# Performance work log

Measured on AMD Instinct MI355X. Metric: run time of the kernel, lower is better.

The kernel has to match this reference:

```python
import jax, jax.numpy as jnp
import numpy as np

BN_EPS = 1e-6
LN_EPS = 1e-5
ROPE_BASE = 10000.0


def rope(x):
    # x: [..., S, d] ; standard half-split rotary embedding, positions 0..S-1
    S, d = x.shape[-2], x.shape[-1]
    half = d // 2
    inv_freq = 1.0 / (ROPE_BASE ** (jnp.arange(half, dtype=jnp.float32) / half))
    ang = jnp.arange(S, dtype=jnp.float32)[:, None] * inv_freq[None, :]  # [S, half]
    cos, sin = jnp.cos(ang), jnp.sin(ang)
    x1, x2 = x[..., :half], x[..., half:]
    return jnp.concatenate([x1 * cos - x2 * sin, x1 * sin + x2 * cos], axis=-1)


def layernorm(x, g, b):
    m = jnp.mean(x, axis=-1, keepdims=True)
    v = jnp.mean((x - m) ** 2, axis=-1, keepdims=True)
    return (x - m) * jax.lax.rsqrt(v + LN_EPS) * g + b


def rms_batchnorm(x, g, b, running):
    # eval-mode RMSBatchNorm1D: normalize by running RMS^2 buffer
    return x * jax.lax.rsqrt(running + BN_EPS) * g + b


def setup_inputs() -> dict:
    B, S, C, H, QD, KD, VD = 4, 2048, 1536, 8, 128, 128, 192
    key = jax.random.key(0)
    ks = jax.random.split(key, 8)
    sc = 0.02
    return {
        'x': jax.random.normal(ks[0], (B, S, C), dtype=jnp.float32),
        'rms_g': jnp.ones((C,), jnp.float32),
        'rms_b': jnp.zeros((C,), jnp.float32),
        'rms_r': jnp.ones((C,), jnp.float32),
        'Wq': jax.random.normal(ks[1], (H * QD, C), jnp.float32) * sc,
        'Wk': jax.random.normal(ks[2], (KD, C), jnp.float32) * sc,
        'Wv': jax.random.normal(ks[3], (VD, C), jnp.float32) * sc,
        'q_g': jnp.ones((QD,), jnp.float32), 'q_b': jnp.zeros((QD,), jnp.float32),
        'k_g': jnp.ones((KD,), jnp.float32), 'k_b': jnp.zeros((KD,), jnp.float32),
        'v_g': jnp.ones((VD,), jnp.float32), 'v_b': jnp.zeros((VD,), jnp.float32),
        'Wo': jax.random.normal(ks[4], (C, H * VD), jnp.float32) * sc,
        'bo': jnp.zeros((C,), jnp.float32),
        'on_g': jnp.ones((C,), jnp.float32),
        'on_b': jnp.zeros((C,), jnp.float32),
        'on_r': jnp.ones((C,), jnp.float32),
    }


def reference(x, rms_g, rms_b, rms_r, Wq, Wk, Wv, q_g, q_b, k_g, k_b, v_g, v_b, Wo, bo, on_g, on_b, on_r):
    B, S, C = x.shape
    H, QD = 8, Wq.shape[0] // 8
    KD, VD = Wk.shape[0], Wv.shape[0]

    xn = rms_batchnorm(x, rms_g, rms_b, rms_r)

    q = (xn @ Wq.T).reshape(B, S, H, QD)       # [B,S,H,QD]
    q = layernorm(q, q_g, q_b)
    k = layernorm(xn @ Wk.T, k_g, k_b)          # [B,S,KD] shared across heads (MQA)
    v = layernorm(xn @ Wv.T, v_g, v_b)          # [B,S,VD]

    # RoPE along sequence dim
    q = rope(jnp.transpose(q, (0, 2, 1, 3)))    # [B,H,S,QD]
    k = rope(k)
    v = rope(v)

    scale = 1.0 / jnp.sqrt(jnp.float32(KD))
    logits = jnp.einsum('bhsc,bSc->bhsS', q, k) * scale   # [B,H,S,S]
    attn = jax.nn.softmax(logits, axis=-1)
    o = jnp.einsum('bhsS,bSc->bshc', attn, v).reshape(B, S, H * VD)

    y = o @ Wo.T + bo                            # [B,S,C]
    y = rms_batchnorm(y, on_g, on_b, on_r)
    # dropout is identity in eval mode
    return y
```

## Files before the change

### kernel.cpp

```cpp
#include <hip/hip_runtime.h>
#include <math.h>

typedef unsigned short u16;
typedef unsigned int   u32;
typedef __attribute__((ext_vector_type(8))) short bf16x8;
typedef __attribute__((ext_vector_type(4))) float f32x4;

#define DEVI static __device__ __forceinline__

constexpr int Bb = 4, Ss = 2048, Cc = 1536, Hh = 8, QD = 128, KD = 128, VD = 192;
constexpr int NTOK = Bb * Ss;
constexpr int NQKV = Hh*QD + KD + VD;
constexpr int NQKV_PAD = 1408;
constexpr float ATTN_SCALE = 0.08838834764831845f;

constexpr size_t OFF_S1  = 0;
constexpr size_t OFF_B1  = OFF_S1 + Cc*4;
constexpr size_t OFF_S2  = OFF_B1 + Cc*4;
constexpr size_t OFF_B2  = OFF_S2 + Cc*4;
constexpr size_t OFF_CT  = 24576;
constexpr size_t OFF_ST  = OFF_CT  + (size_t)Ss*64*4;
constexpr size_t OFF_CTV = OFF_ST  + (size_t)Ss*64*4;
constexpr size_t OFF_STV = OFF_CTV + (size_t)Ss*96*4;
constexpr size_t OFF_WQKV= OFF_STV + (size_t)Ss*96*4;
constexpr size_t OFF_WO  = OFF_WQKV+ (size_t)NQKV_PAD*Cc*2;
constexpr size_t OFF_XN  = OFF_WO  + (size_t)Cc*Cc*2;
constexpr size_t OFF_QKV = OFF_XN  + (size_t)NTOK*Cc*2;
constexpr size_t OFF_Q   = OFF_QKV + (size_t)NTOK*NQKV*2;
constexpr size_t OFF_K   = OFF_Q   + (size_t)NTOK*(Hh*QD)*2;
constexpr size_t OFF_VT  = OFF_K   + (size_t)NTOK*KD*2;

DEVI u16 f2b(float f) {
  union { float f; u32 u; } v; v.f = f;
  u32 r = v.u + 0x7FFFu + ((v.u >> 16) & 1u);
  return (u16)(r >> 16);
}
DEVI float b2f(u16 h) {
  union { u32 u; float f; } v; v.u = ((u32)h) << 16;
  return v.f;
}
DEVI u32 cvtpk(float lo, float hi) {
  u32 r;
  asm("v_cvt_pk_bf16_f32 %0, %1, %2" : "=v"(r) : "v"(lo), "v"(hi));
  return r;
}
DEVI void gload16(const void* g, void* l) {
  __builtin_amdgcn_global_load_lds(g, l, 16, 0, 0);
}
DEVI f32x4 mfma16(bf16x8 a, bf16x8 b, f32x4 c) {
  return __builtin_amdgcn_mfma_f32_16x16x32_bf16(a, b, c, 0, 0, 0);
}

__global__ __launch_bounds__(256) void k_prep_small(
    const float* __restrict__ rms_g, const float* __restrict__ rms_b, const float* __restrict__ rms_r,
    const float* __restrict__ on_g,  const float* __restrict__ on_b,  const float* __restrict__ on_r,
    const float* __restrict__ bo, char* __restrict__ ws)
{
  int i = blockIdx.x * 256 + threadIdx.x;
  float* s1 = (float*)(ws + OFF_S1);
  float* b1 = (float*)(ws + OFF_B1);
  float* s2 = (float*)(ws + OFF_S2);
  float* b2 = (float*)(ws + OFF_B2);
  float* ct = (float*)(ws + OFF_CT);
  float* st = (float*)(ws + OFF_ST);
  float* ctv= (float*)(ws + OFF_CTV);
  float* stv= (float*)(ws + OFF_STV);
  if (i < Cc) {
    float a = rsqrtf(rms_r[i] + 1e-6f) * rms_g[i];
    s1[i] = a; b1[i] = rms_b[i];
    float c = rsqrtf(on_r[i] + 1e-6f) * on_g[i];
    s2[i] = c; b2[i] = bo[i]*c + on_b[i];
  }
  int j = i - Cc;
  if (j >= 0 && j < Ss*64) {
    int s = j >> 6, f = j & 63;
    float invf = expf(-(float)f * (9.210340371976184f / 64.f));
    float ang = (float)s * invf;
    float sn, cs; sincosf(ang, &sn, &cs);
    ct[j] = cs; st[j] = sn;
  }
  int k = j - Ss*64;
  if (k >= 0 && k < Ss*96) {
    int s = k / 96, f = k - s*96;
    float invf = expf(-(float)f * (9.210340371976184f / 96.f));
    float ang = (float)s * invf;
    float sn, cs; sincosf(ang, &sn, &cs);
    ctv[k] = cs; stv[k] = sn;
  }
}

__global__ __launch_bounds__(256) void k_prep_w(
    const float* __restrict__ Wq, const float* __restrict__ Wk, const float* __restrict__ Wv,
    const float* __restrict__ Wo, char* __restrict__ ws)
{
  u16* wqkv = (u16*)(ws + OFF_WQKV);
  u16* wo   = (u16*)(ws + OFF_WO);
  const int total1 = NQKV_PAD * Cc;
  const int total2 = Cc * Cc;
  for (int i = blockIdx.x*256 + threadIdx.x; i < total1 + total2; i += gridDim.x*256) {
    if (i < total1) {
      int r = i / Cc, c = i - r*Cc;
      float v = 0.f;
      if (r < 1024)      v = Wq[(size_t)r*Cc + c];
      else if (r < 1152) v = Wk[(size_t)(r-1024)*Cc + c];
      else if (r < 1344) v = Wv[(size_t)(r-1152)*Cc + c];
      wqkv[i] = f2b(v);
    } else {
      int t2 = i - total1;
      wo[t2] = f2b(Wo[t2]);
    }
  }
}

__global__ __launch_bounds__(256) void k_xn(const float* __restrict__ x, char* __restrict__ ws)
{
  const float* s1 = (const float*)(ws + OFF_S1);
  const float* b1 = (const float*)(ws + OFF_B1);
  u16* xn = (u16*)(ws + OFF_XN);
  int idx = blockIdx.x*256 + threadIdx.x;
  float4 xv = ((const float4*)x)[idx];
  int c = (idx % (Cc/4)) * 4;
  u32 lo = (u32)f2b(xv.x*s1[c]   + b1[c])   | ((u32)f2b(xv.y*s1[c+1] + b1[c+1]) << 16);
  u32 hi = (u32)f2b(xv.z*s1[c+2] + b1[c+2]) | ((u32)f2b(xv.w*s1[c+3] + b1[c+3]) << 16);
  ((uint2*)xn)[idx] = make_uint2(lo, hi);
}

template <bool EPI>
__global__ __launch_bounds__(256) void k_gemm_bt(
    const u16* __restrict__ A, const u16* __restrict__ Bw, void* __restrict__ outp,
    int K, int N_out, const float* __restrict__ s2, const float* __restrict__ b2)
{
  __shared__ u16 a_lds[128*32];
  __shared__ u16 b_lds[128*32];
  const int tid = threadIdx.x;
  const int w = tid >> 6, l = tid & 63;
  const int wr = w >> 1, wc = w & 1;
  const int lr = l & 15, lh = l >> 4;
  const int m0 = blockIdx.y * 128, n0 = blockIdx.x * 128;
  f32x4 acc[4][4] = {};
  const u16* pa = A  + (size_t)(m0 + w*16 + (l>>2))*K + (l&3)*8;
  const u16* pb = Bw + (size_t)(n0 + w*16 + (l>>2))*K + (l&3)*8;
  char* al = (char*)a_lds + w*1024;
  char* bl = (char*)b_lds + w*1024;
  const u16* ar = a_lds + (wr*64 + lr)*32 + lh*8;
  const u16* br = b_lds + (wc*64 + lr)*32 + lh*8;
  for (int k0 = 0; k0 < K; k0 += 32) {
    gload16(pa,                al);
    gload16(pa + (size_t)64*K, al + 4096);
    gload16(pb,                bl);
    gload16(pb + (size_t)64*K, bl + 4096);
    pa += 32; pb += 32;
    __syncthreads();
    bf16x8 af[4], bfr[4];
#pragma unroll
    for (int m = 0; m < 4; m++) af[m]  = *(const bf16x8*)(ar + m*512);
#pragma unroll
    for (int n = 0; n < 4; n++) bfr[n] = *(const bf16x8*)(br + n*512);
#pragma unroll
    for (int m = 0; m < 4; m++)
#pragma unroll
      for (int n = 0; n < 4; n++)
        acc[m][n] = mfma16(af[m], bfr[n], acc[m][n]);
    __syncthreads();
  }
  const int r0 = m0 + wr*64 + lh*4;
  const int c0 = n0 + wc*64 + lr;
#pragma unroll
  for (int m = 0; m < 4; m++) {
#pragma unroll
    for (int n = 0; n < 4; n++) {
      int col = c0 + n*16;
      if (col < N_out) {
#pragma unroll
        for (int r = 0; r < 4; r++) {
          size_t o = (size_t)(r0 + m*16 + r) * N_out + col;
          if (EPI) ((float*)outp)[o] = acc[m][n][r] * s2[col] + b2[col];
          else     ((u16*)outp)[o]   = f2b(acc[m][n][r]);
        }
      }
    }
  }
}

__global__ __launch_bounds__(256) void k_lnrope_qk(
    char* __restrict__ ws,
    const float* __restrict__ q_g, const float* __restrict__ q_b,
    const float* __restrict__ k_g, const float* __restrict__ k_b)
{
  const u16* qkv = (const u16*)(ws + OFF_QKV);
  u16* qo = (u16*)(ws + OFF_Q);
  u16* ko = (u16*)(ws + OFF_K);
  const float* ct = (const float*)(ws + OFF_CT);
  const float* st = (const float*)(ws + OFF_ST);
  const int w = threadIdx.x >> 6, l = threadIdx.x & 63;
  const int rid = blockIdx.x*4 + w;
  const u16* src; u16* dst; const float* g; const float* bb; float osc; int s;
  if (rid < NTOK*Hh) {
    int t = rid >> 3, h = rid & 7;
    s = t & (Ss-1); int b = t >> 11;
    src = qkv + (size_t)t*NQKV + h*QD;
    dst = qo + ((size_t)(b*Hh + h)*Ss + s)*QD;
    g = q_g; bb = q_b; osc = ATTN_SCALE;
  } else {
    int t = rid - NTOK*Hh;
    s = t & (Ss-1);
    src = qkv + (size_t)t*NQKV + Hh*QD;
    dst = ko + (size_t)t*KD;
    g = k_g; bb = k_b; osc = 1.f;
  }
  u32 pk = *(const u32*)(src + 2*l);
  float x0 = b2f((u16)(pk & 0xFFFFu)), x1 = b2f((u16)(pk >> 16));
  float sm = x0 + x1, sq = x0*x0 + x1*x1;
#pragma unroll
  for (int off = 1; off < 64; off <<= 1) { sm += __shfl_xor(sm, off); sq += __shfl_xor(sq, off); }
  float mean = sm * (1.f/128.f);
  float var  = sq * (1.f/128.f) - mean*mean;
  float rstd = rsqrtf(var + 1e-5f);
  int d0 = 2*l;
  float y0 = (x0 - mean)*rstd*g[d0]   + bb[d0];
  float y1 = (x1 - mean)*rstd*g[d0+1] + bb[d0+1];
  float z0 = __shfl_xor(y0, 32);
  float z1 = __shfl_xor(y1, 32);
  int f0 = 2*(l & 31);
  float c0 = ct[s*64 + f0],     s0 = st[s*64 + f0];
  float c1 = ct[s*64 + f0 + 1], s1 = st[s*64 + f0 + 1];
  float o0, o1;
  if (l < 32) { o0 = y0*c0 - z0*s0; o1 = y1*c1 - z1*s1; }
  else        { o0 = z0*s0 + y0*c0; o1 = z1*s1 + y1*c1; }
  o0 *= osc; o1 *= osc;
  *(u32*)(dst + 2*l) = (u32)f2b(o0) | ((u32)f2b(o1) << 16);
}

__global__ __launch_bounds__(256) void k_lnrope_v(
    char* __restrict__ ws, const float* __restrict__ v_g, const float* __restrict__ v_b)
{
  const u16* qkv = (const u16*)(ws + OFF_QKV);
  u16* vo = (u16*)(ws + OFF_VT);
  const float* ct = (const float*)(ws + OFF_CTV);
  const float* st = (const float*)(ws + OFF_STV);
  __shared__ float buf[4][192];
  const int w = threadIdx.x >> 6, l = threadIdx.x & 63;
  const int t = blockIdx.x*4 + w;
  const int s = t & (Ss-1), b = t >> 11;
  const u16* src = qkv + (size_t)t*NQKV + Hh*QD + KD;
  float xs[3]; float sm = 0.f, sq = 0.f;
#pragma unroll
  for (int i2 = 0; i2 < 3; i2++) {
    float xv = b2f(src[l + 64*i2]);
    xs[i2] = xv; buf[w][l + 64*i2] = xv;
    sm += xv; sq += xv*xv;
  }
  __threadfence_block();
#pragma unroll
  for (int off = 1; off < 64; off <<= 1) { sm += __shfl_xor(sm, off); sq += __shfl_xor(sq, off); }
  float mean = sm * (1.f/192.f);
  float var  = sq * (1.f/192.f) - mean*mean;
  float rstd = rsqrtf(var + 1e-5f);
#pragma unroll
  for (int i2 = 0; i2 < 3; i2++) {
    int e = l + 64*i2;
    float val;
    if (e < 96) {
      float x1 = xs[i2], x2 = buf[w][e+96];
      float x1n = (x1-mean)*rstd*v_g[e]    + v_b[e];
      float x2n = (x2-mean)*rstd*v_g[e+96] + v_b[e+96];
      float cs = ct[s*96 + e], sn = st[s*96 + e];
      val = x1n*cs - x2n*sn;
    } else {
      int f = e - 96;
      float x2 = xs[i2], x1 = buf[w][f];
      float x1n = (x1-mean)*rstd*v_g[f] + v_b[f];
      float x2n = (x2-mean)*rstd*v_g[e] + v_b[e];
      float cs = ct[s*96 + f], sn = st[s*96 + f];
      val = x1n*sn + x2n*cs;
    }
    vo[((size_t)b*VD + e)*Ss + s] = f2b(val);
  }
}

__global__ __launch_bounds__(256, 2) void k_attn(const char* __restrict__ ws, u16* __restrict__ O)
{
  const u16* qs = (const u16*)(ws + OFF_Q);
  const u16* ks = (const u16*)(ws + OFF_K);
  const u16* vt = (const u16*)(ws + OFF_VT);
  __shared__ u16 k_lds[64*128];
  __shared__ u16 v_lds[192*64];
  __shared__ u16 p_lds[4][32][72];
  const int tid = threadIdx.x, w = tid >> 6, l = tid & 63;
  const int lr = l & 15, lh = l >> 4;
  const int bid0 = blockIdx.x;
  const int sw = (bid0 & 7)*64 + (bid0 >> 3);
  const int qt = sw & 15, h = (sw >> 4) & 7, b = sw >> 7;
  const int q0 = qt*128 + w*32;
  bf16x8 aq[2][4];
  const u16* qbase = qs + ((size_t)(b*Hh + h)*Ss + q0 + lr)*QD + lh*8;
#pragma unroll
  for (int h2 = 0; h2 < 2; h2++)
#pragma unroll
    for (int kk = 0; kk < 4; kk++)
      aq[h2][kk] = *(const bf16x8*)(qbase + (size_t)h2*16*QD + kk*32);
  float m[2] = {-INFINITY, -INFINITY}, sume[2] = {0.f, 0.f};
  f32x4 acc[2][12] = {};
  const char* ksrc0 = (const char*)(ks + (size_t)b*Ss*KD);
  const char* vsrc0 = (const char*)(vt + (size_t)b*VD*Ss);
  for (int kv0 = 0; kv0 < Ss; kv0 += 64) {
    {
      const char* ksrc = ksrc0 + (size_t)kv0*KD*2;
#pragma unroll
      for (int r = 0; r < 4; r++) {
        int o = r*4096 + w*1024 + l*16;
        gload16(ksrc + (o ^ (((o>>8)&7)<<4)), (char*)k_lds + r*4096 + w*1024);
      }
#pragma unroll
      for (int r = 0; r < 6; r++) {
        int o = r*4096 + w*1024 + l*16;
        int vd = o >> 7, c = o & 127;
        gload16(vsrc0 + (size_t)vd*(Ss*2) + kv0*2 + (c ^ ((vd&7)<<4)),
                (char*)v_lds + r*4096 + w*1024);
      }
    }
    __syncthreads();
    f32x4 sv[2][4] = {};
#pragma unroll
    for (int nt = 0; nt < 4; nt++) {
#pragma unroll
      for (int kk = 0; kk < 4; kk++) {
        int kb = ((nt*16 + lr) << 8) + kk*64 + lh*16;
        kb ^= (lr & 7) << 4;
        bf16x8 bk = *(const bf16x8*)((const char*)k_lds + kb);
        sv[0][nt] = mfma16(bk, aq[0][kk], sv[0][nt]);
        sv[1][nt] = mfma16(bk, aq[1][kk], sv[1][nt]);
      }
    }
#pragma unroll
    for (int h2 = 0; h2 < 2; h2++) {
      float tmx = -INFINITY;
#pragma unroll
      for (int nt = 0; nt < 4; nt++)
        tmx = fmaxf(tmx, fmaxf(fmaxf(sv[h2][nt][0], sv[h2][nt][1]),
                               fmaxf(sv[h2][nt][2], sv[h2][nt][3])));
      tmx = fmaxf(tmx, __shfl_xor(tmx, 16));
      tmx = fmaxf(tmx, __shfl_xor(tmx, 32));
      if (!__all(tmx - m[h2] <= 8.f)) {
        float mnew = fmaxf(m[h2], tmx);
        float scl = __expf(m[h2] - mnew);
        m[h2] = mnew; sume[h2] *= scl;
#pragma unroll
        for (int n = 0; n < 12; n++) acc[h2][n] *= scl;
      }
      float tsum = 0.f;
#pragma unroll
      for (int nt = 0; nt < 4; nt++) {
#pragma unroll
        for (int r2 = 0; r2 < 4; r2++) {
          float e = __expf(sv[h2][nt][r2] - m[h2]);
          sv[h2][nt][r2] = e; tsum += e;
        }
      }
      tsum += __shfl_xor(tsum, 16);
      tsum += __shfl_xor(tsum, 32);
      sume[h2] += tsum;
#pragma unroll
      for (int nt = 0; nt < 4; nt++) {
        u32 w0 = cvtpk(sv[h2][nt][0], sv[h2][nt][1]);
        u32 w1 = cvtpk(sv[h2][nt][2], sv[h2][nt][3]);
        *(u32*)&p_lds[w][h2*16 + lr][nt*16 + lh*4]     = w0;
        *(u32*)&p_lds[w][h2*16 + lr][nt*16 + lh*4 + 2] = w1;
      }
    }
    asm volatile("s_waitcnt lgkmcnt(0)" ::: "memory");
    __builtin_amdgcn_sched_barrier(0);
#pragma unroll
    for (int kk2 = 0; kk2 < 2; kk2++) {
      bf16x8 pb0 = *(const bf16x8*)(&p_lds[w][lr][kk2*32 + lh*8]);
      bf16x8 pb1 = *(const bf16x8*)(&p_lds[w][16 + lr][kk2*32 + lh*8]);
#pragma unroll
      for (int n = 0; n < 12; n++) {
        int vb = ((n*16 + lr) << 7) + kk2*64 + lh*16;
        vb ^= (lr & 7) << 4;
        bf16x8 av = *(const bf16x8*)((const char*)v_lds + vb);
        acc[0][n] = mfma16(av, pb0, acc[0][n]);
        acc[1][n] = mfma16(av, pb1, acc[1][n]);
      }
    }
    __syncthreads();
  }
#pragma unroll
  for (int h2 = 0; h2 < 2; h2++) {
    float inv = 1.f / sume[h2];
#pragma unroll
    for (int n = 0; n < 12; n++) {
      u32 w0 = cvtpk(acc[h2][n][0]*inv, acc[h2][n][1]*inv);
      u32 w1 = cvtpk(acc[h2][n][2]*inv, acc[h2][n][3]*inv);
      size_t o = ((size_t)b*Ss + q0 + h2*16 + lr)*Cc + h*VD + n*16 + lh*4;
      *(uint2*)(O + o) = make_uint2(w0, w1);
    }
  }
}

extern "C" void kernel_launch(void* const* d_in, const int* in_sizes, int n_in,
                              void* d_out, int out_size, void* d_ws, size_t ws_size,
                              hipStream_t stream)
{
  const float* x     = (const float*)d_in[0];
  const float* rms_g = (const float*)d_in[1];
  const float* rms_b = (const float*)d_in[2];
  const float* rms_r = (const float*)d_in[3];
  const float* Wq    = (const float*)d_in[4];
  const float* Wk    = (const float*)d_in[5];
  const float* Wv    = (const float*)d_in[6];
  const float* q_g   = (const float*)d_in[7];
  const float* q_b   = (const float*)d_in[8];
  const float* k_g   = (const float*)d_in[9];
  const float* k_b   = (const float*)d_in[10];
  const float* v_g   = (const float*)d_in[11];
  const float* v_b   = (const float*)d_in[12];
  const float* Wo    = (const float*)d_in[13];
  const float* bo    = (const float*)d_in[14];
  const float* on_g  = (const float*)d_in[15];
  const float* on_b  = (const float*)d_in[16];
  const float* on_r  = (const float*)d_in[17];
  char* ws = (char*)d_ws;

  k_prep_small<<<dim3((Cc + Ss*64 + Ss*96) / 256), 256, 0, stream>>>(
      rms_g, rms_b, rms_r, on_g, on_b, on_r, bo, ws);
  k_prep_w<<<dim3(2048), 256, 0, stream>>>(Wq, Wk, Wv, Wo, ws);
  k_xn<<<dim3(NTOK*Cc/4/256), 256, 0, stream>>>(x, ws);
  k_gemm_bt<false><<<dim3(NQKV_PAD/128, NTOK/128), 256, 0, stream>>>(
      (const u16*)(ws + OFF_XN), (const u16*)(ws + OFF_WQKV), (void*)(ws + OFF_QKV),
      Cc, NQKV, nullptr, nullptr);
  k_lnrope_qk<<<dim3((NTOK*Hh + NTOK)/4), 256, 0, stream>>>(ws, q_g, q_b, k_g, k_b);
  k_lnrope_v<<<dim3(NTOK/4), 256, 0, stream>>>(ws, v_g, v_b);
  k_attn<<<dim3(Bb*Hh*(Ss/128)), 256, 0, stream>>>(ws, (u16*)(ws + OFF_XN));
  k_gemm_bt<true><<<dim3(Cc/128, NTOK/128), 256, 0, stream>>>(
      (const u16*)(ws + OFF_XN), (const u16*)(ws + OFF_WO), d_out,
      Cc, Cc, (const float*)(ws + OFF_S2), (const float*)(ws + OFF_B2));
}
```

Baseline: 387.8 us.

## Replace GEMM with 256x256 multi-stage pipelined kernel and swizzle attention P tile

Replaces the 128x128 single-buffered GEMM with a 256x256, 512-thread kernel. It uses a 4-deep ring of direct global-to-LDS loads, XOR-swizzled LDS layout, an XCD-aware block remap and raised MFMA priority; the QKV weight padding grows to 1536 so the tile fits. The goal is to hide global load latency and raise data reuse per tile. The attention kernel's P staging buffer drops its row padding in favour of an XOR swizzle to avoid LDS bank conflicts. The trade-offs are 192 blocks for 256 CUs, heavy LDS use, and a fixed vmcnt(12) wait in the last iterations that may not guarantee the current stage has landed.

```diff
diff --git a/kernel.cpp b/kernel.cpp
--- a/kernel.cpp
+++ b/kernel.cpp
@@ -11,7 +11,7 @@
 constexpr int Bb = 4, Ss = 2048, Cc = 1536, Hh = 8, QD = 128, KD = 128, VD = 192;
 constexpr int NTOK = Bb * Ss;
 constexpr int NQKV = Hh*QD + KD + VD;
-constexpr int NQKV_PAD = 1408;
+constexpr int NQKV_PAD = 1536;
 constexpr float ATTN_SCALE = 0.08838834764831845f;
 
 constexpr size_t OFF_S1  = 0;
@@ -50,6 +50,9 @@
 DEVI f32x4 mfma16(bf16x8 a, bf16x8 b, f32x4 c) {
   return __builtin_amdgcn_mfma_f32_16x16x32_bf16(a, b, c, 0, 0, 0);
 }
+DEVI int swz64(int byte) {
+  return byte ^ ((((byte>>7)&1)<<4) | (((byte>>8)&1)<<5));
+}
 
 __global__ __launch_bounds__(256) void k_prep_small(
     const float* __restrict__ rms_g, const float* __restrict__ rms_b, const float* __restrict__ rms_r,
@@ -126,56 +129,86 @@
 }
 
 template <bool EPI>
-__global__ __launch_bounds__(256) void k_gemm_bt(
+__global__ __launch_bounds__(512, 2) void k_gemm256(
     const u16* __restrict__ A, const u16* __restrict__ Bw, void* __restrict__ outp,
-    int K, int N_out, const float* __restrict__ s2, const float* __restrict__ b2)
-{
-  __shared__ u16 a_lds[128*32];
-  __shared__ u16 b_lds[128*32];
+    int K, int N_store, const float* __restrict__ s2, const float* __restrict__ b2)
+{
+  __shared__ u16 tiles[4][2][8192];
   const int tid = threadIdx.x;
-  const int w = tid >> 6, l = tid & 63;
-  const int wr = w >> 1, wc = w & 1;
+  const int wid = tid >> 6, l = tid & 63;
   const int lr = l & 15, lh = l >> 4;
-  const int m0 = blockIdx.y * 128, n0 = blockIdx.x * 128;
-  f32x4 acc[4][4] = {};
-  const u16* pa = A  + (size_t)(m0 + w*16 + (l>>2))*K + (l&3)*8;
-  const u16* pb = Bw + (size_t)(n0 + w*16 + (l>>2))*K + (l&3)*8;
-  char* al = (char*)a_lds + w*1024;
-  char* bl = (char*)b_lds + w*1024;
-  const u16* ar = a_lds + (wr*64 + lr)*32 + lh*8;
-  const u16* br = b_lds + (wc*64 + lr)*32 + lh*8;
-  for (int k0 = 0; k0 < K; k0 += 32) {
-    gload16(pa,                al);
-    gload16(pa + (size_t)64*K, al + 4096);
-    gload16(pb,                bl);
-    gload16(pb + (size_t)64*K, bl + 4096);
-    pa += 32; pb += 32;
-    __syncthreads();
-    bf16x8 af[4], bfr[4];
-#pragma unroll
-    for (int m = 0; m < 4; m++) af[m]  = *(const bf16x8*)(ar + m*512);
-#pragma unroll
-    for (int n = 0; n < 4; n++) bfr[n] = *(const bf16x8*)(br + n*512);
-#pragma unroll
-    for (int m = 0; m < 4; m++)
-#pragma unroll
-      for (int n = 0; n < 4; n++)
-        acc[m][n] = mfma16(af[m], bfr[n], acc[m][n]);
-    __syncthreads();
-  }
-  const int r0 = m0 + wr*64 + lh*4;
+  const int wr = wid >> 2, wc = wid & 3;
+  const int id  = blockIdx.x + gridDim.x * blockIdx.y;
+  const int cpx = (gridDim.x * gridDim.y) >> 3;
+  const int sw  = (id & 7) * cpx + (id >> 3);
+  const int by  = sw / gridDim.x;
+  const int bx  = sw - by * gridDim.x;
+  const int m0 = by * 256, n0 = bx * 256;
+
+  const size_t Kb = (size_t)K * 2;
+  const char* aBase = (const char*)(A  + (size_t)m0 * K);
+  const char* bBase = (const char*)(Bw + (size_t)n0 * K);
+  const int o0    = wid*1024 + l*16;
+  const int sfl   = swz64(o0);
+  const size_t srowb = (size_t)(sfl >> 6) * Kb;
+  const int scolb = sfl & 63;
+  int aoff[8], boff[4];
+#pragma unroll
+  for (int mi = 0; mi < 8; mi++) aoff[mi] = swz64((wr*128 + mi*16 + lr)*64 + lh*16);
+#pragma unroll
+  for (int ni = 0; ni < 4; ni++) boff[ni] = swz64((wc*64  + ni*16 + lr)*64 + lh*16);
+
+  f32x4 acc[8][4] = {};
+  const int NT = K >> 5;
+
+#define STAGE(t) {                                                        \
+    char* la_ = (char*)tiles[(t) & 3][0] + wid*1024;                      \
+    char* lb_ = (char*)tiles[(t) & 3][1] + wid*1024;                      \
+    const char* ga_ = aBase + srowb + (size_t)(t)*64 + scolb;             \
+    const char* gb_ = bBase + srowb + (size_t)(t)*64 + scolb;             \
+    gload16(ga_,            la_);                                         \
+    gload16(ga_ + 128*Kb,   la_ + 8192);                                  \
+    gload16(gb_,            lb_);                                         \
+    gload16(gb_ + 128*Kb,   lb_ + 8192);                                  \
+  }
+
+  STAGE(0); STAGE(1); STAGE(2);
+  for (int t = 0; t < NT; ++t) {
+    if (t + 3 < NT) STAGE(t + 3);
+    asm volatile("s_waitcnt vmcnt(12)" ::: "memory");
+    __builtin_amdgcn_s_barrier();
+    const char* la = (const char*)tiles[t & 3][0];
+    const char* lb = (const char*)tiles[t & 3][1];
+    bf16x8 af[8], bfr[4];
+#pragma unroll
+    for (int mi = 0; mi < 8; mi++) af[mi]  = *(const bf16x8*)(la + aoff[mi]);
+#pragma unroll
+    for (int ni = 0; ni < 4; ni++) bfr[ni] = *(const bf16x8*)(lb + boff[ni]);
+    __builtin_amdgcn_s_setprio(1);
+#pragma unroll
+    for (int mi = 0; mi < 8; mi++)
+#pragma unroll
+      for (int ni = 0; ni < 4; ni++)
+        acc[mi][ni] = mfma16(af[mi], bfr[ni], acc[mi][ni]);
+    __builtin_amdgcn_s_setprio(0);
+    asm volatile("s_waitcnt lgkmcnt(0)" ::: "memory");
+    __builtin_amdgcn_s_barrier();
+  }
+#undef STAGE
+
+  const int r0 = m0 + wr*128 + lh*4;
   const int c0 = n0 + wc*64 + lr;
 #pragma unroll
-  for (int m = 0; m < 4; m++) {
-#pragma unroll
-    for (int n = 0; n < 4; n++) {
-      int col = c0 + n*16;
-      if (col < N_out) {
+  for (int mi = 0; mi < 8; mi++) {
+#pragma unroll
+    for (int ni = 0; ni < 4; ni++) {
+      int col = c0 + ni*16;
+      if (col < N_store) {
 #pragma unroll
         for (int r = 0; r < 4; r++) {
-          size_t o = (size_t)(r0 + m*16 + r) * N_out + col;
-          if (EPI) ((float*)outp)[o] = acc[m][n][r] * s2[col] + b2[col];
-          else     ((u16*)outp)[o]   = f2b(acc[m][n][r]);
+          size_t o = (size_t)(r0 + mi*16 + r) * N_store + col;
+          if (EPI) ((float*)outp)[o] = acc[mi][ni][r] * s2[col] + b2[col];
+          else     ((u16*)outp)[o]   = f2b(acc[mi][ni][r]);
         }
       }
     }
@@ -285,7 +318,7 @@
   const u16* vt = (const u16*)(ws + OFF_VT);
   __shared__ u16 k_lds[64*128];
   __shared__ u16 v_lds[192*64];
-  __shared__ u16 p_lds[4][32][72];
+  __shared__ u16 p_lds[4][32][64];
   const int tid = threadIdx.x, w = tid >> 6, l = tid & 63;
   const int lr = l & 15, lh = l >> 4;
   const int bid0 = blockIdx.x;
@@ -360,20 +393,25 @@
       tsum += __shfl_xor(tsum, 16);
       tsum += __shfl_xor(tsum, 32);
       sume[h2] += tsum;
-#pragma unroll
-      for (int nt = 0; nt < 4; nt++) {
-        u32 w0 = cvtpk(sv[h2][nt][0], sv[h2][nt][1]);
-        u32 w1 = cvtpk(sv[h2][nt][2], sv[h2][nt][3]);
-        *(u32*)&p_lds[w][h2*16 + lr][nt*16 + lh*4]     = w0;
-        *(u32*)&p_lds[w][h2*16 + lr][nt*16 + lh*4 + 2] = w1;
+      {
+        char* pw = (char*)&p_lds[w][h2*16 + lr][0];
+#pragma unroll
+        for (int nt = 0; nt < 4; nt++) {
+          u32 w0 = cvtpk(sv[h2][nt][0], sv[h2][nt][1]);
+          u32 w1 = cvtpk(sv[h2][nt][2], sv[h2][nt][3]);
+          int pcol = (nt*32 + lh*8) ^ ((lr & 7) << 4);
+          *(u32*)(pw + pcol)     = w0;
+          *(u32*)(pw + pcol + 4) = w1;
+        }
       }
     }
     asm volatile("s_waitcnt lgkmcnt(0)" ::: "memory");
     __builtin_amdgcn_sched_barrier(0);
 #pragma unroll
     for (int kk2 = 0; kk2 < 2; kk2++) {
-      bf16x8 pb0 = *(const bf16x8*)(&p_lds[w][lr][kk2*32 + lh*8]);
-      bf16x8 pb1 = *(const bf16x8*)(&p_lds[w][16 + lr][kk2*32 + lh*8]);
+      int rcol = (kk2*64 + lh*16) ^ ((lr & 7) << 4);
+      bf16x8 pb0 = *(const bf16x8*)((const char*)&p_lds[w][lr][0]      + rcol);
+      bf16x8 pb1 = *(const bf16x8*)((const char*)&p_lds[w][16 + lr][0] + rcol);
 #pragma unroll
       for (int n = 0; n < 12; n++) {
         int vb = ((n*16 + lr) << 7) + kk2*64 + lh*16;
@@ -426,13 +464,13 @@
       rms_g, rms_b, rms_r, on_g, on_b, on_r, bo, ws);
   k_prep_w<<<dim3(2048), 256, 0, stream>>>(Wq, Wk, Wv, Wo, ws);
   k_xn<<<dim3(NTOK*Cc/4/256), 256, 0, stream>>>(x, ws);
-  k_gemm_bt<false><<<dim3(NQKV_PAD/128, NTOK/128), 256, 0, stream>>>(
+  k_gemm256<false><<<dim3(NQKV_PAD/256, NTOK/256), 512, 0, stream>>>(
       (const u16*)(ws + OFF_XN), (const u16*)(ws + OFF_WQKV), (void*)(ws + OFF_QKV),
       Cc, NQKV, nullptr, nullptr);
   k_lnrope_qk<<<dim3((NTOK*Hh + NTOK)/4), 256, 0, stream>>>(ws, q_g, q_b, k_g, k_b);
   k_lnrope_v<<<dim3(NTOK/4), 256, 0, stream>>>(ws, v_g, v_b);
   k_attn<<<dim3(Bb*Hh*(Ss/128)), 256, 0, stream>>>(ws, (u16*)(ws + OFF_XN));
-  k_gemm_bt<true><<<dim3(Cc/128, NTOK/128), 256, 0, stream>>>(
+  k_gemm256<true><<<dim3(Cc/256, NTOK/256), 512, 0, stream>>>(
       (const u16*)(ws + OFF_XN), (const u16*)(ws + OFF_WO), d_out,
       Cc, Cc, (const float*)(ws + OFF_S2), (const float*)(ws + OFF_B2));
 }
```

New measurement: 374.1 us. 1.04x faster.
